# Kernel tuning notes

Hardware: AMD Instinct MI355X
Metric: run time of the kernel (lower is better)

The kernel has to match this reference:

```python
import jax, jax.numpy as jnp
import numpy as np

B, T, E, H = 2, 2048, 1024, 16
D = E // H


def setup_inputs() -> dict:
    key = jax.random.key(0)
    ks = jax.random.split(key, 8)
    k = jax.random.normal(ks[0], (B, T, E), dtype=jnp.float32)
    q = jax.random.normal(ks[1], (B, T, E), dtype=jnp.float32)
    v = jax.random.normal(ks[2], (B, T, E), dtype=jnp.float32)
    # torch Linear weights: [out, in]; y = x @ W.T (+ b)
    Wk = jax.random.normal(ks[3], (E, E), dtype=jnp.float32) * 0.02
    Wq = jax.random.normal(ks[4], (E, E), dtype=jnp.float32) * 0.02
    Wv = jax.random.normal(ks[5], (E, E), dtype=jnp.float32) * 0.02
    Wo = jax.random.normal(ks[6], (E, E), dtype=jnp.float32) * 0.02
    bo = jax.random.normal(ks[7], (E,), dtype=jnp.float32) * 0.02
    # causal mask: True = masked (as in masked_fill)
    mask = jnp.triu(jnp.ones((T, T), dtype=bool), k=1)
    return {"k": k, "q": q, "v": v, "Wk": Wk, "Wq": Wq, "Wv": Wv,
            "Wo": Wo, "bo": bo, "mask": mask}


def _split_heads(x):  # [b,t,(h d)] -> [b,h,t,d]
    b, t, _ = x.shape
    return x.reshape(b, t, H, D).transpose(0, 2, 1, 3)


def reference(k, q, v, Wk, Wq, Wv, Wo, bo, mask):
    keys = _split_heads(k @ Wk.T)      # no bias (add_bias_kv=False)
    queries = _split_heads(q @ Wq.T)   # q_prj has bias=False always
    values = _split_heads(v @ Wv.T)
    # scores [b,h,t,t]; original applies mask (-inf) then divides by sqrt(d)
    att = jnp.einsum('bhqd,bhkd->bhqk', queries, keys)
    att = jnp.where(mask, -jnp.inf, att)
    att = jax.nn.softmax(att / jnp.sqrt(jnp.float32(D)), axis=-1)
    out = jnp.einsum('bhqk,bhkd->bhqd', att, values)
    out = out.transpose(0, 2, 1, 3).reshape(B, T, E)  # merge heads
    return out @ Wo.T + bo
```

## Files before the change

### kernel.cpp

```cpp
#include <hip/hip_runtime.h>
#include <stdint.h>

typedef __bf16 bf16;
typedef bf16 bf16x8 __attribute__((ext_vector_type(8)));
typedef bf16 bf16x4 __attribute__((ext_vector_type(4)));
typedef float f32x4 __attribute__((ext_vector_type(4)));
typedef float f32x16 __attribute__((ext_vector_type(16)));
typedef unsigned int uint;
typedef uint u32x4 __attribute__((ext_vector_type(4)));

#define MFMA16(a, b, c) __builtin_amdgcn_mfma_f32_16x16x32_bf16(a, b, c, 0, 0, 0)
#define MFMA32(a, b, c) __builtin_amdgcn_mfma_f32_32x32x16_bf16(a, b, c, 0, 0, 0)

static constexpr int Bsz = 2, T = 2048, E = 1024, H = 16, Dh = 64;
static constexpr float QSCALE = 0.125f * 1.44269504088896f;

__device__ __forceinline__ float exp2fast(float x) {
#if __has_builtin(__builtin_amdgcn_exp2f)
    return __builtin_amdgcn_exp2f(x);
#else
    return exp2f(x);
#endif
}

__device__ __forceinline__ void gll16(const bf16* g, bf16* l) {
    __builtin_amdgcn_global_load_lds((const __attribute__((address_space(1))) uint*)g,
                                     (__attribute__((address_space(3))) uint*)l, 16, 0, 0);
}

template <int ROWS>
__device__ __forceinline__ void stage_b16(bf16* lds, const bf16* g, int ldg, int wave, int lane) {
    const int rsub = lane >> 3;
    const int csw = (lane & 7) ^ rsub;
#pragma unroll
    for (int i = 0; i < ROWS / 32; ++i) {
        const int row = wave * (ROWS / 4) + i * 8;
        gll16(g + (size_t)(row + rsub) * ldg + csw * 8, lds + row * 64);
    }
}
__device__ __forceinline__ bf16x8 frag_b16(const bf16* lds, int r, int cc) {
    return *(const bf16x8*)(lds + r * 64 + ((cc ^ (r & 7)) << 3));
}

template <int ROWS>
__device__ __forceinline__ void stage_f32lds(float* lds, const float* g, int ldg,
                                             int wave, int lane) {
    const int rsub = lane >> 4;
#pragma unroll
    for (int i = 0; i < ROWS / 16; ++i) {
        const int slab = wave * (ROWS / 16) + i;
        const int row0 = slab * 4;
        const int src = (lane & 15) ^ ((((slab & 3)) << 2) | rsub);
        gll16((const bf16*)(g + (size_t)(row0 + rsub) * ldg + src * 4),
              (bf16*)(lds + row0 * 64));
    }
}
__device__ __forceinline__ bf16x8 frag_f32(const float* lds, int r, int lc0) {
    const f32x4 u0 = *(const f32x4*)(lds + r * 64 + ((lc0 ^ (r & 15)) << 2));
    const f32x4 u1 = *(const f32x4*)(lds + r * 64 + (((lc0 + 1) ^ (r & 15)) << 2));
    bf16x8 a = {(bf16)u0.x, (bf16)u0.y, (bf16)u0.z, (bf16)u0.w,
                (bf16)u1.x, (bf16)u1.y, (bf16)u1.z, (bf16)u1.w};
    return a;
}

template <bool AF32, bool BF32, int MF, int NF, bool OUTF32>
__device__ __forceinline__ void gemm_body(char* smem, const void* Ap, const void* Bp,
                                          bf16* Yb, float* Yf, const float* bias,
                                          int m0, int n0, int K, int ldy, float oscale) {
    constexpr int BM = MF * 32, BN = NF * 32;
    constexpr int ASZ = BM * 64 * (AF32 ? 4 : 2);
    const int tid = threadIdx.x, lane = tid & 63, wave = tid >> 6;
    const int wm = wave >> 1, wn = wave & 1;
    const int fr = lane & 15, kg16 = lane >> 4;

    f32x4 acc[MF][NF] = {};

    for (int k0 = 0; k0 < K; k0 += 64) {
        if constexpr (AF32)
            stage_f32lds<BM>((float*)smem, (const float*)Ap + (size_t)m0 * K + k0, K, wave, lane);
        else
            stage_b16<BM>((bf16*)smem, (const bf16*)Ap + (size_t)m0 * K + k0, K, wave, lane);
        if constexpr (BF32)
            stage_f32lds<BN>((float*)(smem + ASZ), (const float*)Bp + (size_t)n0 * K + k0,
                             K, wave, lane);
        else
            stage_b16<BN>((bf16*)(smem + ASZ), (const bf16*)Bp + (size_t)n0 * K + k0,
                          K, wave, lane);
        __syncthreads();
#pragma unroll
        for (int kk = 0; kk < 64; kk += 32) {
            bf16x8 af[MF], bfr[NF];
#pragma unroll
            for (int f = 0; f < MF; ++f) {
                const int r = wm * (BM / 2) + f * 16 + fr;
                if constexpr (AF32)
                    af[f] = frag_f32((const float*)smem, r, (kk >> 2) + (kg16 << 1));
                else
                    af[f] = frag_b16((const bf16*)smem, r, (kk >> 3) + kg16);
            }
#pragma unroll
            for (int f = 0; f < NF; ++f) {
                const int r = wn * (BN / 2) + f * 16 + fr;
                if constexpr (BF32)
                    bfr[f] = frag_f32((const float*)(smem + ASZ), r, (kk >> 2) + (kg16 << 1));
                else
                    bfr[f] = frag_b16((const bf16*)(smem + ASZ), r, (kk >> 3) + kg16);
            }
#pragma unroll
            for (int mf = 0; mf < MF; ++mf)
#pragma unroll
                for (int nf = 0; nf < NF; ++nf)
                    acc[mf][nf] = MFMA16(af[mf], bfr[nf], acc[mf][nf]);
        }
        __syncthreads();
    }
    const int rb = (lane >> 4) << 2;
#pragma unroll
    for (int mf = 0; mf < MF; ++mf)
#pragma unroll
        for (int nf = 0; nf < NF; ++nf) {
            int n = n0 + wn * (BN / 2) + nf * 16 + fr;
            float bn = 0.f;
            if constexpr (OUTF32) bn = bias[n];
#pragma unroll
            for (int r = 0; r < 4; ++r) {
                int mm = m0 + wm * (BM / 2) + mf * 16 + rb + r;
                float v = acc[mf][nf][r];
                if constexpr (OUTF32)
                    Yf[(size_t)mm * ldy + n] = v + bn;
                else
                    Yb[(size_t)mm * ldy + n] = (bf16)(v * oscale);
            }
        }
}

__global__ __launch_bounds__(256) void cvt_w(const float* Wq, const float* Wk,
                                             const float* Wv, const float* Wo,
                                             bf16* Wqc, bf16* Wkc, bf16* Wvc, bf16* Woc) {
    const size_t NW = (size_t)E * E;
    const size_t nwork = (4 * NW) >> 2;
    for (size_t t = (size_t)blockIdx.x * 256 + threadIdx.x; t < nwork;
         t += (size_t)gridDim.x * 256) {
        size_t i = t << 2;
        size_t w = i / NW;
        size_t off = i - w * NW;
        const float* s = w == 0 ? Wq : (w == 1 ? Wk : (w == 2 ? Wv : Wo));
        bf16* d = w == 0 ? Wqc : (w == 1 ? Wkc : (w == 2 ? Wvc : Woc));
        const float4 x = *(const float4*)(s + off);
        bf16x4 y = {(bf16)x.x, (bf16)x.y, (bf16)x.z, (bf16)x.w};
        *(bf16x4*)(d + off) = y;
    }
}

template <bool PB>
__global__ __launch_bounds__(256) void qkv_proj(
    const float* q32, const float* k32, const float* v32,
    const bf16* Wq16, const bf16* Wk16, const bf16* Wv16,
    const float* Wq32, const float* Wk32, const float* Wv32,
    bf16* Qb, bf16* Kb, bf16* Vt) {
    __shared__ __align__(16) char smem[PB ? 48 * 1024 : 64 * 1024];
    const int bid = blockIdx.x;
    const int wid = (bid & 7) * 96 + (bid >> 3);
    if (wid < 512) {
        int s = wid >> 8;
        int t = wid & 255;
        int m0 = (t >> 3) * 128, n0 = (t & 7) * 128;
        if constexpr (PB)
            gemm_body<true, false, 4, 4, false>(smem, s ? k32 : q32, s ? Wk16 : Wq16,
                                                s ? Kb : Qb, nullptr, nullptr, m0, n0, E, E,
                                                s ? 1.0f : QSCALE);
        else
            gemm_body<true, true, 4, 4, false>(smem, s ? k32 : q32, s ? Wk32 : Wq32,
                                               s ? Kb : Qb, nullptr, nullptr, m0, n0, E, E,
                                               s ? 1.0f : QSCALE);
    } else {
        int r = wid - 512;
        int b = r >> 7, rr = r & 127;
        int m0 = (rr >> 4) * 128, n0 = (rr & 15) * 128;
        if constexpr (PB)
            gemm_body<false, true, 4, 4, false>(smem, Wv16, v32 + (size_t)b * T * E,
                                                Vt + (size_t)b * E * T, nullptr, nullptr,
                                                m0, n0, E, T, 1.0f);
        else
            gemm_body<true, true, 4, 4, false>(smem, Wv32, v32 + (size_t)b * T * E,
                                               Vt + (size_t)b * E * T, nullptr, nullptr,
                                               m0, n0, E, T, 1.0f);
    }
}

template <bool PB>
__global__ __launch_bounds__(256) void out_proj(const bf16* Xb, const bf16* W16,
                                                const float* W32, float* Y,
                                                const float* bias) {
    __shared__ __align__(16) char smem[PB ? 24 * 1024 : 40 * 1024];
    const int bid = blockIdx.x;
    const int wid = (bid & 7) * 64 + (bid >> 3);
    const int m0 = (wid >> 3) * 64, n0 = (wid & 7) * 128;
    if constexpr (PB)
        gemm_body<false, false, 2, 4, true>(smem, Xb, W16, nullptr, Y, bias, m0, n0, E, E, 1.0f);
    else
        gemm_body<false, true, 2, 4, true>(smem, Xb, W32, nullptr, Y, bias, m0, n0, E, E, 1.0f);
}

__device__ __forceinline__ uint pkbf(float a, float b) {
    uint16_t x = __builtin_bit_cast(uint16_t, (bf16)a);
    uint16_t y = __builtin_bit_cast(uint16_t, (bf16)b);
    return (uint)x | ((uint)y << 16);
}

template <int DMODE>
__device__ __forceinline__ void attn_tile64(const bf16* KL, const bf16* VL,
                                            int l31, int hi, int swz,
                                            const bf16x8 (&qf)[4],
                                            f32x16& o0, f32x16& o1, float& m, float& l) {
    constexpr int NCC = (DMODE == 2) ? 2 : 4;
    f32x16 s0 = {}, s1 = {};
    {
        bf16x8 kf[4];
#pragma unroll
        for (int t = 0; t < 4; ++t)
            kf[t] = *(const bf16x8*)(KL + l31 * 64 + ((((t << 1) | hi) ^ swz) << 3));
        __builtin_amdgcn_s_setprio(1);
#pragma unroll
        for (int t = 0; t < 4; ++t) s0 = MFMA32(kf[t], qf[t], s0);
        __builtin_amdgcn_s_setprio(0);
    }
    if constexpr (DMODE != 2) {
        bf16x8 kf[4];
#pragma unroll
        for (int t = 0; t < 4; ++t)
            kf[t] = *(const bf16x8*)(KL + (32 + l31) * 64 + ((((t << 1) | hi) ^ swz) << 3));
        __builtin_amdgcn_s_setprio(1);
#pragma unroll
        for (int t = 0; t < 4; ++t) s1 = MFMA32(kf[t], qf[t], s1);
        __builtin_amdgcn_s_setprio(0);
    }
    bf16x8 vfa[NCC], vfb[NCC];
#pragma unroll
    for (int cc = 0; cc < NCC; ++cc) {
        vfa[cc] = *(const bf16x8*)(VL + l31 * 64 + ((((cc << 1) | hi) ^ swz) << 3));
        vfb[cc] = *(const bf16x8*)(VL + (32 + l31) * 64 + ((((cc << 1) | hi) ^ swz) << 3));
    }
    if constexpr (DMODE == 2) {
#pragma unroll
        for (int r = 0; r < 16; ++r) {
            int key = (r & 3) + 8 * (r >> 2) + 4 * hi;
            if (key > l31) s0[r] = -1e30f;
        }
    }
    if constexpr (DMODE == 1) {
#pragma unroll
        for (int r = 0; r < 16; ++r) {
            int key = (r & 3) + 8 * (r >> 2) + 4 * hi;
            if (key > l31) s1[r] = -1e30f;
        }
    }
    float t8[8];
    if constexpr (DMODE == 2) {
#pragma unroll
        for (int r = 0; r < 8; ++r) t8[r] = fmaxf(s0[r], s0[r + 8]);
    } else {
#pragma unroll
        for (int r = 0; r < 8; ++r)
            t8[r] = fmaxf(fmaxf(s0[r], s0[r + 8]), fmaxf(s1[r], s1[r + 8]));
    }
#pragma unroll
    for (int r = 0; r < 4; ++r) t8[r] = fmaxf(t8[r], t8[r + 4]);
    float pm = fmaxf(fmaxf(t8[0], t8[1]), fmaxf(t8[2], t8[3]));
    pm = fmaxf(pm, __shfl_xor(pm, 32, 64));

    if (!__all(pm - m <= 11.5f)) {
        float mn = fmaxf(m, pm);
        float al = exp2fast(m - mn);
        m = mn;
        l *= al;
#pragma unroll
        for (int r = 0; r < 16; ++r) {
            int qr = (r & 3) + 8 * (r >> 2) + 4 * hi;
            float aq = __shfl(al, qr, 64);
            o0[r] *= aq;
            o1[r] *= aq;
        }
    }
#pragma unroll
    for (int r = 0; r < 16; ++r) s0[r] = exp2fast(s0[r] - m);
    if constexpr (DMODE != 2) {
#pragma unroll
        for (int r = 0; r < 16; ++r) s1[r] = exp2fast(s1[r] - m);
    }
    float u8[8];
    if constexpr (DMODE == 2) {
#pragma unroll
        for (int r = 0; r < 8; ++r) u8[r] = s0[r] + s0[r + 8];
    } else {
#pragma unroll
        for (int r = 0; r < 8; ++r) u8[r] = (s0[r] + s0[r + 8]) + (s1[r] + s1[r + 8]);
    }
#pragma unroll
    for (int r = 0; r < 4; ++r) u8[r] = u8[r] + u8[r + 4];
    float ps = (u8[0] + u8[1]) + (u8[2] + u8[3]);
    l += ps + __shfl_xor(ps, 32, 64);

    __builtin_amdgcn_s_setprio(1);
#pragma unroll
    for (int cc = 0; cc < NCC; ++cc) {
        const f32x16& ph = (cc < 2) ? s0 : s1;
        const int bse = (cc & 1) * 8;
        uint x0 = pkbf(ph[bse + 0], ph[bse + 1]);
        uint x1 = pkbf(ph[bse + 2], ph[bse + 3]);
        uint y0 = pkbf(ph[bse + 4], ph[bse + 5]);
        uint y1 = pkbf(ph[bse + 6], ph[bse + 7]);
        uint sx0 = __shfl_xor(x0, 32, 64), sx1 = __shfl_xor(x1, 32, 64);
        uint sy0 = __shfl_xor(y0, 32, 64), sy1 = __shfl_xor(y1, 32, 64);
        u32x4 wv;
        wv.x = hi ? sy0 : x0;
        wv.y = hi ? sy1 : x1;
        wv.z = hi ? y0 : sx0;
        wv.w = hi ? y1 : sx1;
        bf16x8 pa = __builtin_bit_cast(bf16x8, wv);
        o0 = MFMA32(pa, vfa[cc], o0);
        o1 = MFMA32(pa, vfb[cc], o1);
    }
    __builtin_amdgcn_s_setprio(0);
}

__global__ __launch_bounds__(256) void attn_fwd(const bf16* __restrict__ Q,
                                                const bf16* __restrict__ K,
                                                const bf16* __restrict__ Vt,
                                                bf16* __restrict__ O) {
    __shared__ __align__(16) bf16 Kl[2][64 * 64];
    __shared__ __align__(16) bf16 Vl[2][64 * 64];

    const int g = blockIdx.x;
    const int lo = g & 255;
    const int xcd = lo & 7, jj = lo >> 3;
    const int hb = xcd * 4 + (jj & 3);
    const int qhi = 15 - (jj >> 2);
    const int qb = (g < 256) ? qhi : 15 - qhi;
    const int h = hb & 15, b = hb >> 4;

    const int tid = threadIdx.x, lane = tid & 63, w = tid >> 6;
    const int l31 = lane & 31, hi = lane >> 5;
    const int q0 = qb * 128 + w * 32;

    const bf16* Qp = Q + (size_t)b * T * E + h * Dh;
    const bf16* Kp = K + (size_t)b * T * E + h * Dh;
    const bf16* Vp = Vt + ((size_t)b * E + h * Dh) * T;

    const int rsub = lane >> 3;
    const int csw = (lane & 7) ^ rsub;
    const int swz = (l31 & 7);

    bf16x8 qf[4];
#pragma unroll
    for (int t = 0; t < 4; ++t)
        qf[t] = *(const bf16x8*)(Qp + (size_t)(q0 + l31) * E + t * 16 + hi * 8);

    f32x16 o0 = {}, o1 = {};
    float m = -1e30f, l = 0.f;
    const int ktD = 2 * qb + (w >> 1);
    const int nK2 = 2 * qb + 2;

#pragma unroll
    for (int ii = 0; ii < 2; ++ii)
        gll16(Kp + (size_t)(16 * w + 8 * ii + rsub) * E + csw * 8, &Kl[0][(2 * w + ii) * 512]);
#pragma unroll
    for (int ii = 0; ii < 2; ++ii)
        gll16(Vp + (size_t)(16 * w + 8 * ii + rsub) * T + csw * 8, &Vl[0][(2 * w + ii) * 512]);

    int cur = 0;
#pragma unroll 1
    for (int K2 = 0; K2 < nK2; ++K2) {
        if (K2 + 1 < nK2) {
            const int kb = (K2 + 1) * 64;
            const bf16* Kg = Kp + (size_t)kb * E;
            const bf16* Vg = Vp + kb;
            bf16* dK = &Kl[cur ^ 1][0];
            bf16* dV = &Vl[cur ^ 1][0];
#pragma unroll
            for (int ii = 0; ii < 2; ++ii)
                gll16(Kg + (size_t)(16 * w + 8 * ii + rsub) * E + csw * 8, dK + (2 * w + ii) * 512);
#pragma unroll
            for (int ii = 0; ii < 2; ++ii)
                gll16(Vg + (size_t)(16 * w + 8 * ii + rsub) * T + csw * 8, dV + (2 * w + ii) * 512);
            asm volatile("s_waitcnt vmcnt(4)" ::: "memory");
        } else {
            asm volatile("s_waitcnt vmcnt(0)" ::: "memory");
        }
        __builtin_amdgcn_s_barrier();
        asm volatile("" ::: "memory");

        const bf16* KL = &Kl[cur][0];
        const bf16* VL = &Vl[cur][0];
        if (K2 < ktD) {
            attn_tile64<0>(KL, VL, l31, hi, swz, qf, o0, o1, m, l);
        } else if (K2 == ktD) {
            if (w & 1)
                attn_tile64<1>(KL, VL, l31, hi, swz, qf, o0, o1, m, l);
            else
                attn_tile64<2>(KL, VL, l31, hi, swz, qf, o0, o1, m, l);
        }
        asm volatile("" ::: "memory");
        __builtin_amdgcn_s_barrier();
        cur ^= 1;
    }

    bf16* Op = O + (size_t)b * T * E + h * Dh;
#pragma unroll
    for (int r = 0; r < 16; ++r) {
        int qr = (r & 3) + 8 * (r >> 2) + 4 * hi;
        float lq = __shfl(l, qr, 64);
        float inv = 1.0f / lq;
        Op[(size_t)(q0 + qr) * E + l31] = (bf16)(o0[r] * inv);
        Op[(size_t)(q0 + qr) * E + 32 + l31] = (bf16)(o1[r] * inv);
    }
}

extern "C" void kernel_launch(void* const* d_in, const int* in_sizes, int n_in,
                              void* d_out, int out_size, void* d_ws, size_t ws_size,
                              hipStream_t stream) {
    const float* k_in = (const float*)d_in[0];
    const float* q_in = (const float*)d_in[1];
    const float* v_in = (const float*)d_in[2];
    const float* Wk = (const float*)d_in[3];
    const float* Wq = (const float*)d_in[4];
    const float* Wv = (const float*)d_in[5];
    const float* Wo = (const float*)d_in[6];
    const float* bo = (const float*)d_in[7];
    float* out = (float*)d_out;

    const size_t NE = (size_t)Bsz * T * E;
    const size_t NW = (size_t)E * E;
    bf16* ws = (bf16*)d_ws;
    bf16* Qb = ws;
    bf16* Kb = ws + NE;
    bf16* Vt = ws + 2 * NE;
    bf16* Ab = ws + 3 * NE;
    bf16* Wqc = ws + 4 * NE;
    bf16* Wkc = Wqc + NW;
    bf16* Wvc = Wkc + NW;
    bf16* Woc = Wvc + NW;

    const bool planB = ws_size >= (4 * NE + 4 * NW) * sizeof(bf16);

    if (planB) {
        cvt_w<<<512, 256, 0, stream>>>(Wq, Wk, Wv, Wo, Wqc, Wkc, Wvc, Woc);
        qkv_proj<true><<<768, 256, 0, stream>>>(q_in, k_in, v_in, Wqc, Wkc, Wvc,
                                                nullptr, nullptr, nullptr, Qb, Kb, Vt);
    } else {
        qkv_proj<false><<<768, 256, 0, stream>>>(q_in, k_in, v_in, nullptr, nullptr, nullptr,
                                                 Wq, Wk, Wv, Qb, Kb, Vt);
    }

    attn_fwd<<<dim3(512), 256, 0, stream>>>(Qb, Kb, Vt, Ab);

    if (planB)
        out_proj<true><<<512, 256, 0, stream>>>(Ab, Woc, nullptr, out, bo);
    else
        out_proj<false><<<512, 256, 0, stream>>>(Ab, nullptr, Wo, out, bo);
}
```

Baseline: 129.5 us.

## Pre-convert activations to bf16 and use double-buffered LDS GEMMs for projections

After: 124.1 us. 4.1% less time.

```diff
diff --git a/kernel.cpp b/kernel.cpp
--- a/kernel.cpp
+++ b/kernel.cpp
@@ -61,6 +61,82 @@
     bf16x8 a = {(bf16)u0.x, (bf16)u0.y, (bf16)u0.z, (bf16)u0.w,
                 (bf16)u1.x, (bf16)u1.y, (bf16)u1.z, (bf16)u1.w};
     return a;
+}
+
+template <int MF, int NF, bool OUTF32>
+__device__ __forceinline__ void gemm_dbuf(bf16* smem, const bf16* A, const bf16* B,
+                                          bf16* Yb, float* Yf, const float* bias,
+                                          int m0, int n0, int K, int ldy, float oscale) {
+    constexpr int BM = MF * 32, BN = NF * 32;
+    constexpr int ABUF = BM * 64, SET = ABUF + BN * 64;
+    const int tid = threadIdx.x, lane = tid & 63, wave = tid >> 6;
+    const int wm = wave >> 1, wn = wave & 1;
+    const int fr = lane & 15, kg16 = lane >> 4;
+
+    f32x4 acc[MF][NF] = {};
+
+    stage_b16<BM>(smem, A + (size_t)m0 * K, K, wave, lane);
+    stage_b16<BN>(smem + ABUF, B + (size_t)n0 * K, K, wave, lane);
+
+    const int NS = K / 64;
+    int cur = 0;
+#pragma unroll 1
+    for (int s = 0; s < NS; ++s) {
+        if (s + 1 < NS) {
+            bf16* dst = smem + (cur ^ 1) * SET;
+            stage_b16<BM>(dst, A + (size_t)m0 * K + (s + 1) * 64, K, wave, lane);
+            stage_b16<BN>(dst + ABUF, B + (size_t)n0 * K + (s + 1) * 64, K, wave, lane);
+            if constexpr (MF + NF == 8)
+                asm volatile("s_waitcnt vmcnt(8)" ::: "memory");
+            else
+                asm volatile("s_waitcnt vmcnt(6)" ::: "memory");
+        } else {
+            asm volatile("s_waitcnt vmcnt(0)" ::: "memory");
+        }
+        __builtin_amdgcn_s_barrier();
+        asm volatile("" ::: "memory");
+
+        const bf16* At = smem + cur * SET;
+        const bf16* Bt = At + ABUF;
+#pragma unroll
+        for (int kk = 0; kk < 64; kk += 32) {
+            bf16x8 af[MF], bfr[NF];
+#pragma unroll
+            for (int f = 0; f < MF; ++f)
+                af[f] = frag_b16(At, wm * (BM / 2) + f * 16 + fr, (kk >> 3) + kg16);
+#pragma unroll
+            for (int f = 0; f < NF; ++f)
+                bfr[f] = frag_b16(Bt, wn * (BN / 2) + f * 16 + fr, (kk >> 3) + kg16);
+            __builtin_amdgcn_s_setprio(1);
+#pragma unroll
+            for (int mf = 0; mf < MF; ++mf)
+#pragma unroll
+                for (int nf = 0; nf < NF; ++nf)
+                    acc[mf][nf] = MFMA16(af[mf], bfr[nf], acc[mf][nf]);
+            __builtin_amdgcn_s_setprio(0);
+        }
+        asm volatile("" ::: "memory");
+        __builtin_amdgcn_s_barrier();
+        cur ^= 1;
+    }
+    const int rb = (lane >> 4) << 2;
+#pragma unroll
+    for (int mf = 0; mf < MF; ++mf)
+#pragma unroll
+        for (int nf = 0; nf < NF; ++nf) {
+            int n = n0 + wn * (BN / 2) + nf * 16 + fr;
+            float bn = 0.f;
+            if constexpr (OUTF32) bn = bias[n];
+#pragma unroll
+            for (int r = 0; r < 4; ++r) {
+                int mm = m0 + wm * (BM / 2) + mf * 16 + rb + r;
+                float v = acc[mf][nf][r];
+                if constexpr (OUTF32)
+                    Yf[(size_t)mm * ldy + n] = v + bn;
+                else
+                    Yb[(size_t)mm * ldy + n] = (bf16)(v * oscale);
+            }
+        }
 }
 
 template <bool AF32, bool BF32, int MF, int NF, bool OUTF32>
@@ -72,9 +148,7 @@
     const int tid = threadIdx.x, lane = tid & 63, wave = tid >> 6;
     const int wm = wave >> 1, wn = wave & 1;
     const int fr = lane & 15, kg16 = lane >> 4;
-
     f32x4 acc[MF][NF] = {};
-
     for (int k0 = 0; k0 < K; k0 += 64) {
         if constexpr (AF32)
             stage_f32lds<BM>((float*)smem, (const float*)Ap + (size_t)m0 * K + k0, K, wave, lane);
@@ -134,72 +208,105 @@
         }
 }
 
-__global__ __launch_bounds__(256) void cvt_w(const float* Wq, const float* Wk,
-                                             const float* Wv, const float* Wo,
-                                             bf16* Wqc, bf16* Wkc, bf16* Wvc, bf16* Woc) {
-    const size_t NW = (size_t)E * E;
-    const size_t nwork = (4 * NW) >> 2;
-    for (size_t t = (size_t)blockIdx.x * 256 + threadIdx.x; t < nwork;
+__global__ __launch_bounds__(256) void cvt_qk(const float* q, const float* k,
+                                              const float* Wq, const float* Wk,
+                                              bf16* qc, bf16* kc, bf16* Wqc, bf16* Wkc) {
+    const size_t NX = (size_t)Bsz * T * E, NW = (size_t)E * E;
+    const size_t n1 = NX, n2 = 2 * NX, n3 = 2 * NX + NW, tot = (2 * NX + 2 * NW) >> 2;
+    for (size_t t = (size_t)blockIdx.x * 256 + threadIdx.x; t < tot;
          t += (size_t)gridDim.x * 256) {
         size_t i = t << 2;
-        size_t w = i / NW;
-        size_t off = i - w * NW;
-        const float* s = w == 0 ? Wq : (w == 1 ? Wk : (w == 2 ? Wv : Wo));
-        bf16* d = w == 0 ? Wqc : (w == 1 ? Wkc : (w == 2 ? Wvc : Woc));
+        const float* s;
+        bf16* d;
+        size_t off;
+        if (i < n1) { s = q; d = qc; off = i; }
+        else if (i < n2) { s = k; d = kc; off = i - n1; }
+        else if (i < n3) { s = Wq; d = Wqc; off = i - n2; }
+        else { s = Wk; d = Wkc; off = i - n3; }
         const float4 x = *(const float4*)(s + off);
         bf16x4 y = {(bf16)x.x, (bf16)x.y, (bf16)x.z, (bf16)x.w};
         *(bf16x4*)(d + off) = y;
     }
 }
-
-template <bool PB>
-__global__ __launch_bounds__(256) void qkv_proj(
+__global__ __launch_bounds__(256) void cvt_vw(const float* v, const float* Wv, const float* Wo,
+                                              bf16* vc, bf16* Wvc, bf16* Woc) {
+    const size_t NX = (size_t)Bsz * T * E, NW = (size_t)E * E;
+    const size_t n1 = NX, n2 = NX + NW, tot = (NX + 2 * NW) >> 2;
+    for (size_t t = (size_t)blockIdx.x * 256 + threadIdx.x; t < tot;
+         t += (size_t)gridDim.x * 256) {
+        size_t i = t << 2;
+        const float* s;
+        bf16* d;
+        size_t off;
+        if (i < n1) { s = v; d = vc; off = i; }
+        else if (i < n2) { s = Wv; d = Wvc; off = i - n1; }
+        else { s = Wo; d = Woc; off = i - n2; }
+        const float4 x = *(const float4*)(s + off);
+        bf16x4 y = {(bf16)x.x, (bf16)x.y, (bf16)x.z, (bf16)x.w};
+        *(bf16x4*)(d + off) = y;
+    }
+}
+
+__global__ __launch_bounds__(256) void proj_qk(const bf16* qc, const bf16* kc,
+                                               const bf16* Wqc, const bf16* Wkc,
+                                               bf16* Qb, bf16* Kb) {
+    __shared__ __align__(16) bf16 smem[2 * (128 * 64 + 128 * 64)];
+    const int bid = blockIdx.x;
+    const int wid = (bid & 7) * 64 + (bid >> 3);
+    const int s = wid >> 8;
+    const int t = wid & 255;
+    const int m0 = (t >> 3) * 128, n0 = (t & 7) * 128;
+    gemm_dbuf<4, 4, false>(smem, s ? kc : qc, s ? Wkc : Wqc, s ? Kb : Qb,
+                           nullptr, nullptr, m0, n0, E, E, s ? 1.0f : QSCALE);
+}
+__global__ __launch_bounds__(256) void proj_v(const bf16* Wvc, const bf16* vc, bf16* Vt) {
+    __shared__ __align__(16) bf16 smem[2 * (128 * 64 + 128 * 64)];
+    const int bid = blockIdx.x;
+    const int wid = (bid & 7) * 32 + (bid >> 3);
+    const int b = wid >> 7, rr = wid & 127;
+    const int m0 = (rr >> 4) * 128, n0 = (rr & 15) * 128;
+    gemm_dbuf<4, 4, false>(smem, Wvc, vc + (size_t)b * T * E, Vt + (size_t)b * E * T,
+                           nullptr, nullptr, m0, n0, E, T, 1.0f);
+}
+__global__ __launch_bounds__(256) void out_proj_db(const bf16* Xb, const bf16* W16,
+                                                   float* Y, const float* bias) {
+    __shared__ __align__(16) bf16 smem[2 * (64 * 64 + 128 * 64)];
+    const int bid = blockIdx.x;
+    const int wid = (bid & 7) * 64 + (bid >> 3);
+    const int m0 = (wid >> 3) * 64, n0 = (wid & 7) * 128;
+    gemm_dbuf<2, 4, true>(smem, Xb, W16, nullptr, Y, bias, m0, n0, E, E, 1.0f);
+}
+
+__global__ __launch_bounds__(256) void qkv_proj_fb(
     const float* q32, const float* k32, const float* v32,
-    const bf16* Wq16, const bf16* Wk16, const bf16* Wv16,
     const float* Wq32, const float* Wk32, const float* Wv32,
     bf16* Qb, bf16* Kb, bf16* Vt) {
-    __shared__ __align__(16) char smem[PB ? 48 * 1024 : 64 * 1024];
+    __shared__ __align__(16) char smem[64 * 1024];
     const int bid = blockIdx.x;
     const int wid = (bid & 7) * 96 + (bid >> 3);
     if (wid < 512) {
         int s = wid >> 8;
         int t = wid & 255;
         int m0 = (t >> 3) * 128, n0 = (t & 7) * 128;
-        if constexpr (PB)
-            gemm_body<true, false, 4, 4, false>(smem, s ? k32 : q32, s ? Wk16 : Wq16,
-                                                s ? Kb : Qb, nullptr, nullptr, m0, n0, E, E,
-                                                s ? 1.0f : QSCALE);
-        else
-            gemm_body<true, true, 4, 4, false>(smem, s ? k32 : q32, s ? Wk32 : Wq32,
-                                               s ? Kb : Qb, nullptr, nullptr, m0, n0, E, E,
-                                               s ? 1.0f : QSCALE);
+        gemm_body<true, true, 4, 4, false>(smem, s ? k32 : q32, s ? Wk32 : Wq32,
+                                           s ? Kb : Qb, nullptr, nullptr, m0, n0, E, E,
+                                           s ? 1.0f : QSCALE);
     } else {
         int r = wid - 512;
         int b = r >> 7, rr = r & 127;
         int m0 = (rr >> 4) * 128, n0 = (rr & 15) * 128;
-        if constexpr (PB)
-            gemm_body<false, true, 4, 4, false>(smem, Wv16, v32 + (size_t)b * T * E,
-                                                Vt + (size_t)b * E * T, nullptr, nullptr,
-                                                m0, n0, E, T, 1.0f);
-        else
-            gemm_body<true, true, 4, 4, false>(smem, Wv32, v32 + (size_t)b * T * E,
-                                               Vt + (size_t)b * E * T, nullptr, nullptr,
-                                               m0, n0, E, T, 1.0f);
-    }
-}
-
-template <bool PB>
-__global__ __launch_bounds__(256) void out_proj(const bf16* Xb, const bf16* W16,
-                                                const float* W32, float* Y,
-                                                const float* bias) {
-    __shared__ __align__(16) char smem[PB ? 24 * 1024 : 40 * 1024];
+        gemm_body<true, true, 4, 4, false>(smem, Wv32, v32 + (size_t)b * T * E,
+                                           Vt + (size_t)b * E * T, nullptr, nullptr,
+                                           m0, n0, E, T, 1.0f);
+    }
+}
+__global__ __launch_bounds__(256) void out_proj_fb(const bf16* Xb, const float* W32,
+                                                   float* Y, const float* bias) {
+    __shared__ __align__(16) char smem[40 * 1024];
     const int bid = blockIdx.x;
     const int wid = (bid & 7) * 64 + (bid >> 3);
     const int m0 = (wid >> 3) * 64, n0 = (wid & 7) * 128;
-    if constexpr (PB)
-        gemm_body<false, false, 2, 4, true>(smem, Xb, W16, nullptr, Y, bias, m0, n0, E, E, 1.0f);
-    else
-        gemm_body<false, true, 2, 4, true>(smem, Xb, W32, nullptr, Y, bias, m0, n0, E, E, 1.0f);
+    gemm_body<false, true, 2, 4, true>(smem, Xb, W32, nullptr, Y, bias, m0, n0, E, E, 1.0f);
 }
 
 __device__ __forceinline__ uint pkbf(float a, float b) {
@@ -444,18 +551,18 @@
     const bool planB = ws_size >= (4 * NE + 4 * NW) * sizeof(bf16);
 
     if (planB) {
-        cvt_w<<<512, 256, 0, stream>>>(Wq, Wk, Wv, Wo, Wqc, Wkc, Wvc, Woc);
-        qkv_proj<true><<<768, 256, 0, stream>>>(q_in, k_in, v_in, Wqc, Wkc, Wvc,
-                                                nullptr, nullptr, nullptr, Qb, Kb, Vt);
+        bf16* qc = Ab;
+        bf16* kc = Vt;
+        bf16* vc = Ab;
+        cvt_qk<<<1024, 256, 0, stream>>>(q_in, k_in, Wq, Wk, qc, kc, Wqc, Wkc);
+        proj_qk<<<512, 256, 0, stream>>>(qc, kc, Wqc, Wkc, Qb, Kb);
+        cvt_vw<<<1024, 256, 0, stream>>>(v_in, Wv, Wo, vc, Wvc, Woc);
+        proj_v<<<256, 256, 0, stream>>>(Wvc, vc, Vt);
+        attn_fwd<<<dim3(512), 256, 0, stream>>>(Qb, Kb, Vt, Ab);
+        out_proj_db<<<512, 256, 0, stream>>>(Ab, Woc, out, bo);
     } else {
-        qkv_proj<false><<<768, 256, 0, stream>>>(q_in, k_in, v_in, nullptr, nullptr, nullptr,
-                                                 Wq, Wk, Wv, Qb, Kb, Vt);
-    }
-
-    attn_fwd<<<dim3(512), 256, 0, stream>>>(Qb, Kb, Vt, Ab);
-
-    if (planB)
-        out_proj<true><<<512, 256, 0, stream>>>(Ab, Woc, nullptr, out, bo);
-    else
-        out_proj<false><<<512, 256, 0, stream>>>(Ab, nullptr, Wo, out, bo);
-}
+        qkv_proj_fb<<<768, 256, 0, stream>>>(q_in, k_in, v_in, Wq, Wk, Wv, Qb, Kb, Vt);
+        attn_fwd<<<dim3(512), 256, 0, stream>>>(Qb, Kb, Vt, Ab);
+        out_proj_fb<<<512, 256, 0, stream>>>(Ab, Wo, out, bo);
+    }
+}
```
